# Kernel optimization log

Hardware: AMD Instinct MI355X
Metric: run time of the kernel (lower is better)

## Reference

```python
import jax, jax.numpy as jnp
import numpy as np

Bsz, T, D = 2, 2048, 1024
H_ATTN, HD, WIN = 16, 64, 128
H_SSM, DI, N, DCONV, DTR = 8, 2048, 16, 4, 64
P = DI // H_SSM
DT_MIN, DT_MAX = 1e-4, 1.0
EPS = 1e-6


def setup_inputs() -> dict:
    key = jax.random.key(0)
    ks = jax.random.split(key, 16)
    def g(i, shp, s=0.02):
        return jax.random.normal(ks[i], shp, jnp.float32) * s
    TOT = 2 * DI + DTR + 2 * H_SSM * N
    # dt_bias = inverse_softplus(dt) with dt log-uniform in [dt_min, dt_max]
    dt0 = jnp.exp(jax.random.uniform(ks[14], (H_SSM,), jnp.float32) * (np.log(DT_MAX) - np.log(DT_MIN)) + np.log(DT_MIN))
    dt_bias = dt0 + jnp.log(-jnp.expm1(-dt0))
    return dict(
        x=jax.random.normal(ks[0], (Bsz, T, D), jnp.float32),
        norm1_w=jnp.ones((D,), jnp.float32),
        norm2_w=jnp.ones((D,), jnp.float32),
        Win=g(1, (TOT, D)),
        Wdt=g(2, (H_SSM, DTR)),
        conv_w=g(3, (DI, DCONV), 0.2),
        conv_b=jnp.zeros((DI,), jnp.float32),
        A_log=jnp.log(jnp.broadcast_to(jnp.arange(1, N + 1, dtype=jnp.float32), (H_SSM, N))),
        Dskip=jnp.ones((H_SSM, P), jnp.float32),
        dt_bias=dt_bias,
        ssd_norm_w=jnp.ones((DI,), jnp.float32),
        Wout_ssd=g(4, (D, DI)),
        Wres=g(5, (DI, D)),
        Wq=g(6, (D, D)), Wk=g(7, (D, D)), Wv=g(8, (D, D)), Wo=g(9, (D, D)),
    )


def _rms(x, w):
    return x * jax.lax.rsqrt(jnp.mean(x * x, -1, keepdims=True) + EPS) * w


def _silu(x):
    return x * jax.nn.sigmoid(x)


def _dwconv(x, w, b):
    # causal depthwise conv1d: x [B,T,C], w [C,K], left-pad K-1
    K = w.shape[1]
    xp = jnp.pad(x, ((0, 0), (K - 1, 0), (0, 0)))
    y = sum(xp[:, k:k + x.shape[1], :] * w[:, k] for k in range(K))
    return y + b


def _rope(q, k):
    # q,k: [B,H,T,HD]
    inv = 1.0 / (10000.0 ** (jnp.arange(0, HD, 2, dtype=jnp.float32) / HD))
    t = jnp.arange(q.shape[2], dtype=jnp.float32)
    f = jnp.concatenate([t[:, None] * inv, t[:, None] * inv], -1)  # [T,HD]
    cos, sin = jnp.cos(f), jnp.sin(f)
    def rot(x):
        h = x.shape[-1] // 2
        return jnp.concatenate([-x[..., h:], x[..., :h]], -1)
    return q * cos + rot(q) * sin, k * cos + rot(k) * sin


def _ssd_branch(u, Win, Wdt, conv_w, conv_b, A_log, Dskip, dt_bias, ssd_norm_w, Wout_ssd, Wres):
    B = u.shape[0]
    proj = u @ Win.T  # [B,T,4416]
    xin = proj[..., :DI]
    z = proj[..., DI:2 * DI]
    dtl = proj[..., 2 * DI:2 * DI + DTR]
    o = 2 * DI + DTR
    Bm = proj[..., o:o + H_SSM * N].reshape(B, T, H_SSM, N)
    Cm = proj[..., o + H_SSM * N:].reshape(B, T, H_SSM, N)
    xc = _silu(_dwconv(xin, conv_w, conv_b))
    dt = jnp.clip(jax.nn.softplus(dtl @ Wdt.T + dt_bias), DT_MIN, DT_MAX)  # [B,T,H]
    A = -jnp.exp(A_log)  # [H,N]
    xh = xc.reshape(B, T, H_SSM, P)
    dA = jnp.exp(dt[..., None] * A)  # [B,T,H,N]
    dtB = dt[..., None] * Bm        # [B,T,H,N]

    def step(h, inp):
        dA_t, dtB_t, x_t, C_t = inp
        h = h * dA_t[:, :, None, :] + x_t[..., None] * dtB_t[:, :, None, :]
        y = jnp.einsum('bhpn,bhn->bhp', h, C_t)
        return h, y

    h0 = jnp.zeros((B, H_SSM, P, N), u.dtype)
    _, ys = jax.lax.scan(step, h0, (
        dA.transpose(1, 0, 2, 3), dtB.transpose(1, 0, 2, 3),
        xh.transpose(1, 0, 2, 3), Cm.transpose(1, 0, 2, 3)))
    y = ys.transpose(1, 0, 2, 3) + Dskip * xh  # [B,T,H,P]
    y = y.reshape(B, T, DI) + u @ Wres.T       # residual_proj(d_model->d_inner)
    y = _rms(y * _silu(z), ssd_norm_w)         # fused gated RMSNorm
    return y @ Wout_ssd.T


def _attn(u, Wq, Wk, Wv, Wo):
    B = u.shape[0]
    q = (u @ Wq.T).reshape(B, T, H_ATTN, HD).transpose(0, 2, 1, 3)
    k = (u @ Wk.T).reshape(B, T, H_ATTN, HD).transpose(0, 2, 1, 3)
    v = (u @ Wv.T).reshape(B, T, H_ATTN, HD).transpose(0, 2, 1, 3)
    q, k = _rope(q, k)
    s = jnp.einsum('bhtd,bhsd->bhts', q, k) / np.sqrt(HD).astype(np.float32)
    rel = jnp.arange(T)[:, None] - jnp.arange(T)[None, :]
    allowed = (rel >= 0) & (rel < WIN)  # causal sliding window
    s = jnp.where(allowed, s, jnp.float32(-1e30))
    p = jax.nn.softmax(s, axis=-1)
    y = jnp.einsum('bhts,bhsd->bhtd', p, v)
    return y.transpose(0, 2, 1, 3).reshape(B, T, D) @ Wo.T


def reference(x, norm1_w, norm2_w, Win, Wdt, conv_w, conv_b, A_log, Dskip, dt_bias,
              ssd_norm_w, Wout_ssd, Wres, Wq, Wk, Wv, Wo):
    h = x + _ssd_branch(_rms(x, norm1_w), Win, Wdt, conv_w, conv_b, A_log, Dskip,
                        dt_bias, ssd_norm_w, Wout_ssd, Wres)
    return h + _attn(_rms(h, norm2_w), Wq, Wk, Wv, Wo)
```

## Files before the change

kernel.cpp:

```cpp
#include <hip/hip_runtime.h>
#include <stdint.h>

typedef unsigned short u16;
typedef unsigned int u32;
typedef __attribute__((ext_vector_type(8))) short short8;
typedef __attribute__((ext_vector_type(4))) unsigned short ushort4v;
typedef __attribute__((ext_vector_type(4))) float f32x4;

#define Bsz 2
#define Tn 2048
#define Dm 1024
#define H_ATTN 16
#define HDx 64
#define WINx 128
#define H_SSM 8
#define DIx 2048
#define Nst 16
#define DTRx 64
#define Px 256
#define TOTx 4416
#define TOT2 6464
#define RESOFF 4416
#define OFFC (2*DIx+DTRx+H_SSM*Nst)
#define BT (Bsz*Tn)
#define NCH 32
#define LCH 64

__device__ __forceinline__ float b2f(u16 u){ u32 x = ((u32)u)<<16; float f; __builtin_memcpy(&f,&x,4); return f; }
__device__ __forceinline__ u16 f2b(float f){ u32 x; __builtin_memcpy(&x,&f,4); u32 r = x + 0x7fffu + ((x>>16)&1u); return (u16)(r>>16); }

__device__ __forceinline__ float block_sum256(float v){
  #pragma unroll
  for (int o=32;o;o>>=1) v += __shfl_xor(v,o,64);
  __shared__ float sb[4];
  int wid = threadIdx.x>>6;
  if ((threadIdx.x&63)==0) sb[wid]=v;
  __syncthreads();
  v = sb[0]+sb[1]+sb[2]+sb[3];
  __syncthreads();
  return v;
}

__device__ __forceinline__ void gload_lds16(const void* g, void* l){
  __builtin_amdgcn_global_load_lds((const __attribute__((address_space(1))) void*)g,
                                   (__attribute__((address_space(3))) void*)l, 16, 0, 0);
}

struct CvtArgs { const float* s[7]; u16* d[7]; int n[7]; };
__global__ __launch_bounds__(256) void k_cvt_all(CvtArgs a, int total4){
  int i = blockIdx.x*256 + threadIdx.x;
  if (i >= total4) return;
  int e = i*4;
  #pragma unroll
  for (int j=0;j<7;j++){
    if (e < a.n[j]){
      float4 v = *(const float4*)(a.s[j]+e);
      u16* d = a.d[j]+e;
      d[0]=f2b(v.x); d[1]=f2b(v.y); d[2]=f2b(v.z); d[3]=f2b(v.w);
      return;
    }
    e -= a.n[j];
  }
}

__global__ __launch_bounds__(256) void k_rms1024(const float* __restrict__ src, const float* __restrict__ w,
                                                 u16* __restrict__ dst){
  int row = blockIdx.x, tid = threadIdx.x;
  const float* s = src + (size_t)row*1024;
  float v[4]; float ss=0.f;
  #pragma unroll
  for (int i=0;i<4;i++){ v[i] = s[tid + i*256]; ss += v[i]*v[i]; }
  ss = block_sum256(ss);
  float sc = rsqrtf(ss*(1.0f/1024.0f) + 1e-6f);
  u16* d = dst + (size_t)row*1024;
  #pragma unroll
  for (int i=0;i<4;i++){ int c = tid+i*256; d[c] = f2b(v[i]*sc*w[c]); }
}

#define BKq 64

__global__ __launch_bounds__(512,1)
void k_gemm256(const u16* __restrict__ A, const u16* __restrict__ W,
               u16* __restrict__ C16, int M, int N, int K, int gxx){
  __shared__ u16 lds[2][4][128*64];
  int tid = threadIdx.x, lane = tid&63, wid = tid>>6;
  int bid = blockIdx.x;
  int xcd = bid&7, r = bid>>3;
  int halfg = gxx>>1;
  int row0 = (xcd>>1)<<2, col0 = (xcd&1)*halfg;
  int bx = col0 + (r>>2), by = row0 + (r&3);
  int bm = by*256, bn = bx*256;
  int wr = wid>>2, wcn = wid&3;
  int fr = lane&15, fq = lane>>4;
  f32x4 acc[2][2][4][2];
  #pragma unroll
  for (int a=0;a<2;a++)
    #pragma unroll
    for (int b=0;b<2;b++)
      #pragma unroll
      for (int c=0;c<4;c++)
        #pragma unroll
        for (int d=0;d<2;d++)
          #pragma unroll
          for (int rr=0;rr<4;rr++) acc[a][b][c][d][rr]=0.f;

  auto stageHalf = [&](int b, int q, int tt){
    int k0 = tt*BKq;
    #pragma unroll
    for (int i=0;i<2;i++){
      int idx = i*512 + tid;
      int row = idx>>3, c8 = idx&7;
      const u16* src; int gr;
      if (q < 2){ gr = bm + q*128 + row;     if (gr > M-1) gr = M-1; src = A; }
      else      { gr = bn + (q-2)*128 + row; if (gr > N-1) gr = N-1; src = W; }
      gload_lds16(src + (size_t)gr*K + k0 + ((c8 ^ (row&7)))*8, &lds[b][q][(size_t)idx*8]);
    }
  };
  auto loadA = [&](const u16* aP, short8 (&af)[2][4]){
    #pragma unroll
    for (int kk=0;kk<2;kk++)
      #pragma unroll
      for (int mi=0;mi<4;mi++){
        int row = wr*64 + mi*16 + fr;
        af[kk][mi] = *(const short8*)(aP + row*64 + ((kk*4+fq) ^ (row&7))*8);
      }
  };
  auto loadB = [&](const u16* bP, short8 (&bf)[2][2]){
    #pragma unroll
    for (int kk=0;kk<2;kk++)
      #pragma unroll
      for (int ni=0;ni<2;ni++){
        int row = wcn*32 + ni*16 + fr;
        bf[kk][ni] = *(const short8*)(bP + row*64 + ((kk*4+fq) ^ (row&7))*8);
      }
  };

  int NT = K/BKq;
  stageHalf(0,0,0); stageHalf(0,2,0); stageHalf(0,3,0); stageHalf(0,1,0);

  short8 af[2][4], bf0[2][2], bf1[2][2];
  for (int t=0;t<NT;t++){
    int cb = t&1, nb = cb^1;
    int tn = (t+1 < NT) ? t+1 : t;
    const u16* A0 = &lds[cb][0][0];
    const u16* A1 = &lds[cb][1][0];
    const u16* B0 = &lds[cb][2][0];
    const u16* B1 = &lds[cb][3][0];
    stageHalf(nb,0,tn);
    asm volatile("s_waitcnt vmcnt(6)" ::: "memory");
    __builtin_amdgcn_sched_barrier(0);
    __builtin_amdgcn_s_barrier();
    loadA(A0, af); loadB(B0, bf0);
    asm volatile("s_waitcnt lgkmcnt(0)" ::: "memory");
    __builtin_amdgcn_sched_barrier(0);
    __builtin_amdgcn_s_setprio(1);
    #pragma unroll
    for (int kk=0;kk<2;kk++)
      #pragma unroll
      for (int mi=0;mi<4;mi++)
        #pragma unroll
        for (int ni=0;ni<2;ni++)
          acc[0][0][mi][ni] = __builtin_amdgcn_mfma_f32_16x16x32_bf16(af[kk][mi], bf0[kk][ni], acc[0][0][mi][ni], 0,0,0);
    __builtin_amdgcn_s_setprio(0);
    __builtin_amdgcn_s_barrier();
    stageHalf(nb,2,tn);
    asm volatile("s_waitcnt vmcnt(6)" ::: "memory");
    __builtin_amdgcn_sched_barrier(0);
    __builtin_amdgcn_s_barrier();
    loadB(B1, bf1);
    asm volatile("s_waitcnt lgkmcnt(0)" ::: "memory");
    __builtin_amdgcn_sched_barrier(0);
    __builtin_amdgcn_s_setprio(1);
    #pragma unroll
    for (int kk=0;kk<2;kk++)
      #pragma unroll
      for (int mi=0;mi<4;mi++)
        #pragma unroll
        for (int ni=0;ni<2;ni++)
          acc[0][1][mi][ni] = __builtin_amdgcn_mfma_f32_16x16x32_bf16(af[kk][mi], bf1[kk][ni], acc[0][1][mi][ni], 0,0,0);
    __builtin_amdgcn_s_setprio(0);
    __builtin_amdgcn_s_barrier();
    stageHalf(nb,3,tn);
    asm volatile("s_waitcnt vmcnt(6)" ::: "memory");
    __builtin_amdgcn_sched_barrier(0);
    __builtin_amdgcn_s_barrier();
    loadA(A1, af);
    asm volatile("s_waitcnt lgkmcnt(0)" ::: "memory");
    __builtin_amdgcn_sched_barrier(0);
    __builtin_amdgcn_s_setprio(1);
    #pragma unroll
    for (int kk=0;kk<2;kk++)
      #pragma unroll
      for (int mi=0;mi<4;mi++)
        #pragma unroll
        for (int ni=0;ni<2;ni++)
          acc[1][1][mi][ni] = __builtin_amdgcn_mfma_f32_16x16x32_bf16(af[kk][mi], bf1[kk][ni], acc[1][1][mi][ni], 0,0,0);
    __builtin_amdgcn_s_setprio(0);
    __builtin_amdgcn_s_barrier();
    stageHalf(nb,1,tn);
    asm volatile("s_waitcnt vmcnt(6)" ::: "memory");
    __builtin_amdgcn_sched_barrier(0);
    __builtin_amdgcn_s_barrier();
    __builtin_amdgcn_s_setprio(1);
    #pragma unroll
    for (int kk=0;kk<2;kk++)
      #pragma unroll
      for (int mi=0;mi<4;mi++)
        #pragma unroll
        for (int ni=0;ni<2;ni++)
          acc[1][0][mi][ni] = __builtin_amdgcn_mfma_f32_16x16x32_bf16(af[kk][mi], bf0[kk][ni], acc[1][0][mi][ni], 0,0,0);
    __builtin_amdgcn_s_setprio(0);
    __builtin_amdgcn_s_barrier();
  }
  #pragma unroll
  for (int mh=0;mh<2;mh++)
    #pragma unroll
    for (int nh=0;nh<2;nh++)
      #pragma unroll
      for (int mi=0;mi<4;mi++)
        #pragma unroll
        for (int ni=0;ni<2;ni++){
          int row0o = bm + mh*128 + wr*64 + mi*16 + fq*4;
          int col  = bn + nh*128 + wcn*32 + ni*16 + fr;
          if (col < N){
            #pragma unroll
            for (int rr=0;rr<4;rr++)
              C16[(size_t)(row0o+rr)*N + col] = f2b(acc[mh][nh][mi][ni][rr]);
          }
        }
}

template<int NWC>
__global__ __launch_bounds__(256, (NWC==2?2:3))
void k_gemm(const u16* __restrict__ A, const u16* __restrict__ W,
            float* __restrict__ C, u16* __restrict__ C16, const u16* __restrict__ ADD16,
            u16* __restrict__ qro, u16* __restrict__ kro, u16* __restrict__ vro,
            int M, int N, int K, int gx, int mode){
  constexpr int BN    = 64*NWC;
  constexpr int ROWS  = 128 + BN;
  constexpr int NLOADS= ROWS/32;
  constexpr int MFRAG = (NWC==2)?4:2;
  __shared__ u16 lds[2][ROWS*64];
  int tid = threadIdx.x, lane = tid&63, wid = tid>>6;
  int nwg = gridDim.x;
  int cpx = nwg>>3;
  int bid = blockIdx.x;
  int swz = (bid&7)*cpx + (bid>>3);
  int fourgx = gx<<2;
  int super = swz / fourgx;
  int r     = swz % fourgx;
  int bx = r >> 2;
  int by = (super<<2) + (r&3);
  int bm = by*128, bn = bx*BN;
  int wc = (NWC==2) ? (wid&1) : 0;
  int wr = (NWC==2) ? (wid>>1) : wid;
  int fr = lane&15, fq = lane>>4;
  int s7 = fr&7;
  f32x4 acc[MFRAG][4];
  #pragma unroll
  for (int mi=0;mi<MFRAG;mi++)
    #pragma unroll
    for (int ni=0;ni<4;ni++)
      #pragma unroll
      for (int rr=0;rr<4;rr++) acc[mi][ni][rr]=0.f;

  auto stage = [&](int buf, int t){
    int k0 = t*BKq;
    #pragma unroll
    for (int i=0;i<NLOADS;i++){
      int chunk = i*256 + tid;
      int row = chunk>>3, c8 = chunk&7;
      const u16* src;
      if (row < 128){ int ra = bm + row; if (ra > M-1) ra = M-1; src = A + (size_t)ra*K; }
      else          { int rb = bn + row-128; if (rb > N-1) rb = N-1; src = W + (size_t)rb*K; }
      gload_lds16(src + k0 + ((c8 ^ (row&7)))*8, &lds[buf][(size_t)chunk*8]);
    }
  };

  int NT = K/BKq;
  stage(0, 0);
  stage(1, 1);
  for (int t=0;t<NT;t++){
    int cur = t&1;
    if (t+1 < NT){
      if constexpr (NWC==2) asm volatile("s_waitcnt vmcnt(8)" ::: "memory");
      else                  asm volatile("s_waitcnt vmcnt(6)" ::: "memory");
    } else {
      asm volatile("s_waitcnt vmcnt(0)" ::: "memory");
    }
    __builtin_amdgcn_sched_barrier(0);
    __builtin_amdgcn_s_barrier();
    #pragma unroll
    for (int kk=0;kk<2;kk++){
      short8 bf4[4], af4[MFRAG];
      int slotb = ((kk*4 + fq) ^ s7)*8;
      #pragma unroll
      for (int ni=0;ni<4;ni++)
        bf4[ni] = *(const short8*)(&lds[cur][(128 + wc*64 + ni*16 + fr)*64 + slotb]);
      #pragma unroll
      for (int mi=0;mi<MFRAG;mi++)
        af4[mi] = *(const short8*)(&lds[cur][(wr*(MFRAG*16) + mi*16 + fr)*64 + slotb]);
      #pragma unroll
      for (int mi=0;mi<MFRAG;mi++)
        #pragma unroll
        for (int ni=0;ni<4;ni++)
          acc[mi][ni] = __builtin_amdgcn_mfma_f32_16x16x32_bf16(af4[mi], bf4[ni], acc[mi][ni], 0,0,0);
    }
    asm volatile("s_waitcnt lgkmcnt(0)" ::: "memory");
    __builtin_amdgcn_sched_barrier(0);
    __builtin_amdgcn_s_barrier();
    if (t+2 < NT) stage(cur, t+2);
  }
  if (mode == 5){
    int sec = bn >> 10;
    int hh  = (bn >> 6) & 15;
    #pragma unroll
    for (int mi=0;mi<MFRAG;mi++){
      #pragma unroll
      for (int rr=0;rr<4;rr++){
        int row = bm + wr*(MFRAG*16) + mi*16 + fq*4 + rr;
        int tt = row & (Tn-1), bb = row >> 11;
        size_t dstb = (((size_t)bb*H_ATTN + hh)*Tn + tt)*64;
        if (sec == 2){
          #pragma unroll
          for (int ni=0;ni<4;ni++)
            vro[dstb + ni*16 + fr] = f2b(acc[mi][ni][rr]);
        } else {
          u16* dst = (sec==0) ? qro : kro;
          #pragma unroll
          for (int ni=0;ni<2;ni++){
            int dh = ni*16 + fr;
            float ang = (float)tt * exp2f(-(float)dh * (13.287712379549449f/32.0f));
            float cs = cosf(ang), sn = sinf(ang);
            float lo = acc[mi][ni][rr], hi = acc[mi][ni+2][rr];
            dst[dstb + dh]      = f2b(lo*cs - hi*sn);
            dst[dstb + dh + 32] = f2b(hi*cs + lo*sn);
          }
        }
      }
    }
    return;
  }
  #pragma unroll
  for (int mi=0;mi<MFRAG;mi++){
    int row0 = bm + wr*(MFRAG*16) + mi*16 + fq*4;
    #pragma unroll
    for (int ni=0;ni<4;ni++){
      int col = bn + wc*64 + ni*16 + fr;
      if (col < N){
        #pragma unroll
        for (int rr=0;rr<4;rr++){
          size_t idx = (size_t)(row0+rr)*N + col;
          float v = acc[mi][ni][rr];
          if (mode == 0)      C[idx] = v;
          else if (mode == 2) C16[idx] = f2b(v);
          else                C[idx] = b2f(ADD16[idx]) + v;
        }
      }
    }
  }
}

__global__ __launch_bounds__(256) void k_scan1(
    const u16* __restrict__ proj, const float* __restrict__ Wdt,
    const float* __restrict__ dt_bias, const float* __restrict__ A_log,
    const float* __restrict__ cw, const float* __restrict__ cb,
    const float* __restrict__ Dskip,
    float* __restrict__ expS, u16* __restrict__ y, float* __restrict__ LS){
  __shared__ float sA[1024], sS[1024], sB[1024], sC[1024];
  int bx = blockIdx.x;
  int c = bx & 31, h = (bx>>5)&7, b = bx>>8;
  int tid = threadIdx.x;
  size_t t0 = (size_t)b*Tn + c*64;
  int j = tid>>2, q = tid&3, n0 = q*4;
  {
    const u16* dtl = proj + (t0+j)*TOT2 + 2*DIx + q*16;
    short8 d0 = *(const short8*)(dtl);
    short8 d1 = *(const short8*)(dtl+8);
    const float* wrow = Wdt + h*64 + q*16;
    float part = 0.f;
    #pragma unroll
    for (int e=0;e<8;e++){ part += b2f((u16)d0[e])*wrow[e]; part += b2f((u16)d1[e])*wrow[8+e]; }
    part += __shfl_xor(part, 1, 64);
    part += __shfl_xor(part, 2, 64);
    float v = part + dt_bias[h];
    float sp = (v > 20.0f) ? v : log1pf(expf(v));
    float dt = fminf(fmaxf(sp, 1e-4f), 1.0f);
    ushort4v bm4 = *(const ushort4v*)(proj + (t0+j)*TOT2 + 2*DIx + DTRx + h*16 + n0);
    ushort4v cm4 = *(const ushort4v*)(proj + (t0+j)*TOT2 + OFFC + h*16 + n0);
    #pragma unroll
    for (int i=0;i<4;i++){
      float Av = -expf(A_log[h*16 + n0 + i]);
      sA[j*16+n0+i] = dt*Av;
      sB[j*16+n0+i] = dt*b2f(bm4[i]);
      sC[j*16+n0+i] = b2f(cm4[i]);
    }
  }
  __syncthreads();
  if (tid < 16){
    float cum = 0.f;
    for (int jj=0;jj<64;jj++){ cum += sA[jj*16+tid]; sS[jj*16+tid] = cum; }
  }
  __syncthreads();
  {
    float e[4], s4[4];
    #pragma unroll
    for (int i=0;i<4;i++){ e[i] = expf(sA[j*16+n0+i]); s4[i] = expf(sS[j*16+n0+i]); }
    #pragma unroll
    for (int i=0;i<4;i++){ sA[j*16+n0+i] = e[i]; sS[j*16+n0+i] = s4[i]; }
    float4 ev; ev.x=s4[0]; ev.y=s4[1]; ev.z=s4[2]; ev.w=s4[3];
    *(float4*)(expS + (t0+j)*128 + h*16 + n0) = ev;
  }
  __syncthreads();
  float st[16];
  #pragma unroll
  for (int n=0;n<16;n++) st[n]=0.f;
  int ch = h*Px + tid;
  const u16* pxin = proj + t0*TOT2 + ch;
  const u16* pres = proj + t0*TOT2 + RESOFF + ch;
  float w0=cw[ch*4+0], w1=cw[ch*4+1], w2=cw[ch*4+2], w3=cw[ch*4+3];
  float bcv = cb[ch];
  float dsk = Dskip[ch];
  float x3=0.f, x2=0.f, x1=0.f;
  if (c > 0){
    x3 = b2f(pxin[-(ptrdiff_t)3*TOT2]);
    x2 = b2f(pxin[-(ptrdiff_t)2*TOT2]);
    x1 = b2f(pxin[-(ptrdiff_t)TOT2]);
  }
  u16* yp = y + t0*DIx + ch;
  for (int jj=0;jj<64;jj++){
    float x0 = b2f(pxin[(size_t)jj*TOT2]);
    float cv = bcv + x3*w0 + x2*w1 + x1*w2 + x0*w3;
    float x = cv / (1.0f + expf(-cv));
    x3=x2; x2=x1; x1=x0;
    float acc = b2f(pres[(size_t)jj*TOT2]) + dsk*x;
    #pragma unroll
    for (int n=0;n<16;n++){ st[n] = st[n]*sA[jj*16+n] + x*sB[jj*16+n]; acc += st[n]*sC[jj*16+n]; }
    yp[(size_t)jj*DIx] = f2b(acc);
  }
  float* ls = LS + ((((size_t)b*8+h)*NCH + c)*Px + tid)*16;
  #pragma unroll
  for (int n=0;n<16;n++) ls[n] = st[n];
}

__global__ __launch_bounds__(256) void k_scan2(const float* __restrict__ expS, const float* __restrict__ LS,
                                               float* __restrict__ H0){
  int blk = blockIdx.x;
  int slice = blk & 15;
  int bh = blk >> 4; int b = bh>>3, h = bh&7;
  int tid = threadIdx.x;
  int ch = slice*16 + (tid>>4);
  int n  = tid & 15;
  float Hs = 0.f;
  for (int c=0;c<NCH;c++){
    float dl = expS[((size_t)b*Tn + c*64 + 63)*128 + h*16 + n];
    size_t base = ((((size_t)b*8+h)*NCH + c)*Px + ch)*16 + n;
    H0[base] = Hs;
    Hs = Hs*dl + LS[base];
  }
}

__global__ __launch_bounds__(256) void k_scan3(const u16* __restrict__ proj, const float* __restrict__ expS,
    const float* __restrict__ H0, u16* __restrict__ y){
  __shared__ float ce[1024];
  int bx = blockIdx.x; int c = bx&31, h=(bx>>5)&7, b=bx>>8;
  int tid = threadIdx.x;
  size_t t0 = (size_t)b*Tn + c*64;
  int j = tid>>2, n0=(tid&3)*4;
  {
    ushort4v cv = *(const ushort4v*)(proj + (t0+j)*TOT2 + OFFC + h*16 + n0);
    float4 evv = *(const float4*)(expS + (t0+j)*128 + h*16 + n0);
    ce[j*16+n0+0] = b2f(cv[0])*evv.x; ce[j*16+n0+1] = b2f(cv[1])*evv.y;
    ce[j*16+n0+2] = b2f(cv[2])*evv.z; ce[j*16+n0+3] = b2f(cv[3])*evv.w;
  }
  __syncthreads();
  float h0[16];
  size_t base = ((((size_t)b*8+h)*NCH + c)*Px + tid)*16;
  #pragma unroll
  for (int n=0;n<16;n++) h0[n] = H0[base+n];
  int ch = h*Px + tid;
  u16* yp = y + t0*DIx + ch;
  for (int jj=0;jj<64;jj++){
    float f = 0.f;
    #pragma unroll
    for (int n=0;n<16;n++) f += ce[jj*16+n]*h0[n];
    size_t yi = (size_t)jj*DIx;
    yp[yi] = f2b(b2f(yp[yi]) + f);
  }
}

__global__ __launch_bounds__(256) void k_gatedrms(const u16* __restrict__ y, const u16* __restrict__ proj,
     const float* __restrict__ w, u16* __restrict__ yn){
  int row = blockIdx.x, tid = threadIdx.x;
  const u16* yr = y + (size_t)row*DIx;
  const u16* zr = proj + (size_t)row*TOT2 + DIx;
  float v[8]; float ss=0.f;
  #pragma unroll
  for (int i=0;i<8;i++){
    int cidx = tid + i*256;
    float z = b2f(zr[cidx]);
    float g = b2f(yr[cidx]) * (z / (1.0f + expf(-z)));
    v[i]=g; ss += g*g;
  }
  ss = block_sum256(ss);
  float sc = rsqrtf(ss*(1.0f/2048.0f) + 1e-6f);
  u16* d = yn + (size_t)row*DIx;
  #pragma unroll
  for (int i=0;i<8;i++){ int cidx=tid+i*256; d[cidx] = f2b(v[i]*sc*w[cidx]); }
}

__global__ __launch_bounds__(256) void k_addrms(const float* __restrict__ x, const u16* __restrict__ sout16,
     const float* __restrict__ w, u16* __restrict__ hb16, u16* __restrict__ u2){
  int row=blockIdx.x, tid=threadIdx.x;
  float v[4]; float ss=0.f;
  #pragma unroll
  for (int i=0;i<4;i++){
    int cidx = tid + i*256;
    size_t idx = (size_t)row*1024 + cidx;
    float hv = x[idx] + b2f(sout16[idx]);
    hb16[idx] = f2b(hv);
    v[i]=hv; ss+=hv*hv;
  }
  ss = block_sum256(ss);
  float sc = rsqrtf(ss*(1.0f/1024.0f)+1e-6f);
  #pragma unroll
  for (int i=0;i<4;i++){ int cidx=tid+i*256; u2[(size_t)row*1024+cidx] = f2b(v[i]*sc*w[cidx]); }
}

#define QT 64
#define KSPAN 192
__device__ __forceinline__ u32 swz128a(int row, int b){
  return (u32)((row*128 + b) ^ ((((row&7)^((row>>3)&7)))<<4));
}
__device__ __forceinline__ u32 swz384a(int row, int b){
  return (u32)((row*384 + b) ^ ((((row&7)^((row>>3)&7)))<<4));
}

__global__ __launch_bounds__(256) void k_attn_mfma(const u16* __restrict__ qr, const u16* __restrict__ kr,
    const u16* __restrict__ vr, u16* __restrict__ ya){
  __shared__ u16 bufK[KSPAN*64];
  __shared__ u16 bufV[64*KSPAN];
  int tid = threadIdx.x, lane = tid&63, wid = tid>>6;
  int fr = lane&15, fq = lane>>4;
  int blk = blockIdx.x;
  int qt = blk & 31, bh = blk >> 5;
  int t0 = qt*QT;
  size_t rowbase = (size_t)bh*Tn;
  char* cK = (char*)bufK;
  char* cV = (char*)bufV;

  #pragma unroll
  for (int it=0; it<6; ++it){
    int chunk = it*256 + tid;
    int row = chunk>>3, c8 = chunk&7;
    int sg = t0 - 128 + row;
    if (sg >= 0){
      short8 v = *(const short8*)(kr + (rowbase+sg)*64 + c8*8);
      *(short8*)(cK + swz128a(row, c8*16)) = v;
    }
  }
  #pragma unroll
  for (int it=0; it<6; ++it){
    int idx = it*256 + tid;
    int s = idx>>3, c8 = idx&7, d0 = c8*8;
    int sg = t0 - 128 + s;
    short8 v;
    if (sg >= 0) v = *(const short8*)(vr + (rowbase+sg)*64 + d0);
    else         v = short8{0,0,0,0,0,0,0,0};
    #pragma unroll
    for (int e=0;e<8;e++)
      *(u16*)(cV + swz384a(d0+e, s*2)) = (u16)v[e];
  }
  __syncthreads();

  f32x4 acc[12];
  #pragma unroll
  for (int j=0;j<12;j++)
    #pragma unroll
    for (int r=0;r<4;r++) acc[j][r]=0.f;
  #pragma unroll
  for (int kk=0;kk<2;kk++){
    short8 aq = *(const short8*)(qr + (rowbase + t0 + wid*16 + fr)*64 + kk*32 + fq*8);
    #pragma unroll
    for (int j=0;j<12;j++){
      short8 bk = *(const short8*)(cK + swz128a(j*16+fr, kk*64 + fq*16));
      acc[j] = __builtin_amdgcn_mfma_f32_16x16x32_bf16(aq, bk, acc[j], 0,0,0);
    }
  }

  float p[12][4];
  int cb = lane&15;
  #pragma unroll
  for (int r=0;r<4;r++){
    int rq = wid*16 + (lane>>4)*4 + r;
    float m = -3.0e38f;
    #pragma unroll
    for (int j=0;j<12;j++){
      int c = j*16 + cb;
      bool allowed = (c > rq) && (c <= rq+128) && (c >= 128 - t0);
      float v = allowed ? acc[j][r]*0.125f : -3.0e38f;
      p[j][r] = v;
      m = fmaxf(m, v);
    }
    #pragma unroll
    for (int o=1;o<16;o<<=1) m = fmaxf(m, __shfl_xor(m, o, 64));
    float sum = 0.f;
    #pragma unroll
    for (int j=0;j<12;j++){ float e = __expf(p[j][r]-m); p[j][r]=e; sum += e; }
    #pragma unroll
    for (int o=1;o<16;o<<=1) sum += __shfl_xor(sum, o, 64);
    float inv = 1.0f/sum;
    #pragma unroll
    for (int j=0;j<12;j++) p[j][r] *= inv;
  }
  __syncthreads();

  #pragma unroll
  for (int r=0;r<4;r++){
    int rq = wid*16 + (lane>>4)*4 + r;
    #pragma unroll
    for (int j=0;j<12;j++){
      *(u16*)(cK + swz384a(rq, (j*16+cb)*2)) = f2b(p[j][r]);
    }
  }
  __syncthreads();

  f32x4 acc2[4];
  #pragma unroll
  for (int f=0;f<4;f++)
    #pragma unroll
    for (int r=0;r<4;r++) acc2[f][r]=0.f;
  #pragma unroll
  for (int kk=0;kk<6;kk++){
    short8 ap = *(const short8*)(cK + swz384a(wid*16 + fr, kk*64 + fq*16));
    #pragma unroll
    for (int f=0;f<4;f++){
      short8 bv = *(const short8*)(cV + swz384a(f*16+fr, kk*64 + fq*16));
      acc2[f] = __builtin_amdgcn_mfma_f32_16x16x32_bf16(ap, bv, acc2[f], 0,0,0);
    }
  }
  int b = bh >> 4, h = bh & 15;
  #pragma unroll
  for (int f=0;f<4;f++){
    int d = f*16 + cb;
    #pragma unroll
    for (int r=0;r<4;r++){
      int q = t0 + wid*16 + (lane>>4)*4 + r;
      ya[((size_t)b*Tn + q)*Dm + h*64 + d] = f2b(acc2[f][r]);
    }
  }
}

extern "C" void kernel_launch(void* const* d_in, const int* in_sizes, int n_in,
                              void* d_out, int out_size, void* d_ws, size_t ws_size,
                              hipStream_t stream) {
  const float* x        = (const float*)d_in[0];
  const float* norm1_w  = (const float*)d_in[1];
  const float* norm2_w  = (const float*)d_in[2];
  const float* Win      = (const float*)d_in[3];
  const float* Wdt      = (const float*)d_in[4];
  const float* conv_w   = (const float*)d_in[5];
  const float* conv_b   = (const float*)d_in[6];
  const float* A_log    = (const float*)d_in[7];
  const float* Dskip    = (const float*)d_in[8];
  const float* dt_bias  = (const float*)d_in[9];
  const float* ssd_norm = (const float*)d_in[10];
  const float* Wout_ssd = (const float*)d_in[11];
  const float* Wres     = (const float*)d_in[12];
  const float* Wq       = (const float*)d_in[13];
  const float* Wk       = (const float*)d_in[14];
  const float* Wv       = (const float*)d_in[15];
  const float* Wo       = (const float*)d_in[16];

  char* ws = (char*)d_ws;
  size_t off = 0;
  auto alloc = [&](size_t bytes){ size_t r = off; off += (bytes + 255) & ~(size_t)255; return r; };

  size_t o_WinB  = alloc((size_t)TOTx*Dm*2);
  size_t o_WresB = alloc((size_t)DIx*Dm*2);
  size_t o_WoutB = alloc((size_t)Dm*DIx*2);
  size_t o_WqB   = alloc((size_t)Dm*Dm*2);
  size_t o_WkB   = alloc((size_t)Dm*Dm*2);
  size_t o_WvB   = alloc((size_t)Dm*Dm*2);
  size_t o_WoB   = alloc((size_t)Dm*Dm*2);
  size_t o_u1    = alloc((size_t)BT*Dm*2);
  size_t o_proj  = alloc((size_t)BT*TOT2*2);
  size_t o_sout  = alloc((size_t)BT*Dm*2);
  size_t o_expS  = alloc((size_t)BT*H_SSM*Nst*4);
  size_t o_LS    = alloc((size_t)Bsz*H_SSM*NCH*Px*Nst*4);
  size_t o_H0    = alloc((size_t)Bsz*H_SSM*NCH*Px*Nst*4);
  size_t o_y     = alloc((size_t)BT*DIx*2);
  size_t o_yn    = alloc((size_t)BT*DIx*2);
  size_t o_hb    = alloc((size_t)BT*Dm*2);
  size_t o_qr    = alloc((size_t)Bsz*H_ATTN*Tn*HDx*2);
  size_t o_kr    = alloc((size_t)Bsz*H_ATTN*Tn*HDx*2);

  u16* WinB  = (u16*)(ws + o_WinB);
  u16* WoutB = (u16*)(ws + o_WoutB);
  u16* WqB   = (u16*)(ws + o_WqB);
  u16* u1    = (u16*)(ws + o_u1);
  u16* projb = (u16*)(ws + o_proj);
  float* expS = (float*)(ws + o_expS);
  float* LS   = (float*)(ws + o_LS);
  float* H0   = (float*)(ws + o_H0);
  u16*   ybuf16 = (u16*)(ws + o_y);
  u16*   yn   = (u16*)(ws + o_yn);
  u16*   hb16 = (u16*)(ws + o_hb);
  u16*   sout16 = (u16*)(ws + o_sout);
  u16* qr = (u16*)(ws + o_qr);
  u16* kr = (u16*)(ws + o_kr);
  u16* vr = u1;
  u16* yatt = (u16*)(ws + o_y);

  {
    CvtArgs a;
    a.s[0]=Win;  a.d[0]=WinB;  a.n[0]=TOTx*Dm;
    a.s[1]=Wres; a.d[1]=(u16*)(ws + o_WresB); a.n[1]=DIx*Dm;
    a.s[2]=Wout_ssd; a.d[2]=WoutB; a.n[2]=Dm*DIx;
    a.s[3]=Wq; a.d[3]=WqB; a.n[3]=Dm*Dm;
    a.s[4]=Wk; a.d[4]=(u16*)(ws + o_WkB); a.n[4]=Dm*Dm;
    a.s[5]=Wv; a.d[5]=(u16*)(ws + o_WvB); a.n[5]=Dm*Dm;
    a.s[6]=Wo; a.d[6]=(u16*)(ws + o_WoB); a.n[6]=Dm*Dm;
    int total4 = (a.n[0]+a.n[1]+a.n[2]+a.n[3]+a.n[4]+a.n[5]+a.n[6])/4;
    k_cvt_all<<<dim3((total4+255)/256), dim3(256), 0, stream>>>(a, total4);
  }

  k_rms1024<<<dim3(BT), dim3(256), 0, stream>>>(x, norm1_w, u1);
  k_gemm256<<<dim3(16*26), dim3(512), 0, stream>>>(u1, WinB, projb, BT, TOT2, Dm, 26);
  k_scan1<<<dim3(Bsz*H_SSM*NCH), dim3(256), 0, stream>>>(projb, Wdt, dt_bias, A_log,
                                                         conv_w, conv_b, Dskip, expS, ybuf16, LS);
  k_scan2<<<dim3(Bsz*H_SSM*16), dim3(256), 0, stream>>>(expS, LS, H0);
  k_scan3<<<dim3(Bsz*H_SSM*NCH), dim3(256), 0, stream>>>(projb, expS, H0, ybuf16);
  k_gatedrms<<<dim3(BT), dim3(256), 0, stream>>>(ybuf16, projb, ssd_norm, yn);
  k_gemm<1><<<dim3(16*32), dim3(256), 0, stream>>>(yn, WoutB, nullptr, sout16, nullptr,
                                                   nullptr, nullptr, nullptr, BT, Dm, DIx, 16, 2);
  k_addrms<<<dim3(BT), dim3(256), 0, stream>>>(x, sout16, norm2_w, hb16, (u16*)(ws + o_yn));
  u16* u2p = (u16*)(ws + o_yn);
  k_gemm<1><<<dim3(48*32), dim3(256), 0, stream>>>(u2p, WqB, nullptr, nullptr, nullptr,
                                                   qr, kr, vr, BT, 3*Dm, Dm, 48, 5);
  k_attn_mfma<<<dim3(Bsz*H_ATTN*(Tn/QT)), dim3(256), 0, stream>>>(qr, kr, vr, yatt);
  k_gemm<1><<<dim3(16*32), dim3(256), 0, stream>>>(yatt, (u16*)(ws + o_WoB), (float*)d_out, nullptr, hb16,
                                                   nullptr, nullptr, nullptr, BT, Dm, Dm, 16, 3);
  (void)in_sizes; (void)n_in; (void)out_size; (void)ws_size;
}
```

Baseline: 271.6 us.

## Stage scan inputs through LDS and move residual add into gated RMSNorm

k_scan1 now copies the 64x256 block of conv inputs into shared memory with 16-byte global-to-LDS loads, replacing the strided per-timestep 2-byte global reads. k_scan3 stages its y tile in LDS, updates it there, and writes it back as vectorized short8 stores. The residual projection add moves from scan1 into k_gatedrms, where it is read as coalesced rows. The cost is 32KB of extra LDS per block, which may lower occupancy. The residual is now added after the bf16 rounding of y rather than in fp32 inside the scan, so results can differ slightly.

```diff
diff --git a/kernel.cpp b/kernel.cpp
--- a/kernel.cpp
+++ b/kernel.cpp
@@ -368,11 +368,18 @@
     const float* __restrict__ Dskip,
     float* __restrict__ expS, u16* __restrict__ y, float* __restrict__ LS){
   __shared__ float sA[1024], sS[1024], sB[1024], sC[1024];
+  __shared__ u16 xt[64*256];
   int bx = blockIdx.x;
   int c = bx & 31, h = (bx>>5)&7, b = bx>>8;
   int tid = threadIdx.x;
   size_t t0 = (size_t)b*Tn + c*64;
   int j = tid>>2, q = tid&3, n0 = q*4;
+  #pragma unroll
+  for (int i=0;i<8;i++){
+    int chunk = i*256 + tid;
+    int row = chunk>>5, col8 = (chunk&31)*8;
+    gload_lds16(proj + (t0+row)*TOT2 + h*Px + col8, &xt[(size_t)chunk*8]);
+  }
   {
     const u16* dtl = proj + (t0+j)*TOT2 + 2*DIx + q*16;
     short8 d0 = *(const short8*)(dtl);
@@ -417,7 +424,6 @@
   for (int n=0;n<16;n++) st[n]=0.f;
   int ch = h*Px + tid;
   const u16* pxin = proj + t0*TOT2 + ch;
-  const u16* pres = proj + t0*TOT2 + RESOFF + ch;
   float w0=cw[ch*4+0], w1=cw[ch*4+1], w2=cw[ch*4+2], w3=cw[ch*4+3];
   float bcv = cb[ch];
   float dsk = Dskip[ch];
@@ -429,11 +435,11 @@
   }
   u16* yp = y + t0*DIx + ch;
   for (int jj=0;jj<64;jj++){
-    float x0 = b2f(pxin[(size_t)jj*TOT2]);
+    float x0 = b2f(xt[jj*256 + tid]);
     float cv = bcv + x3*w0 + x2*w1 + x1*w2 + x0*w3;
     float x = cv / (1.0f + expf(-cv));
     x3=x2; x2=x1; x1=x0;
-    float acc = b2f(pres[(size_t)jj*TOT2]) + dsk*x;
+    float acc = dsk*x;
     #pragma unroll
     for (int n=0;n<16;n++){ st[n] = st[n]*sA[jj*16+n] + x*sB[jj*16+n]; acc += st[n]*sC[jj*16+n]; }
     yp[(size_t)jj*DIx] = f2b(acc);
@@ -463,10 +469,17 @@
 __global__ __launch_bounds__(256) void k_scan3(const u16* __restrict__ proj, const float* __restrict__ expS,
     const float* __restrict__ H0, u16* __restrict__ y){
   __shared__ float ce[1024];
+  __shared__ u16 yt[64*256];
   int bx = blockIdx.x; int c = bx&31, h=(bx>>5)&7, b=bx>>8;
   int tid = threadIdx.x;
   size_t t0 = (size_t)b*Tn + c*64;
   int j = tid>>2, n0=(tid&3)*4;
+  #pragma unroll
+  for (int i=0;i<8;i++){
+    int chunk = i*256 + tid;
+    int row = chunk>>5, col8 = (chunk&31)*8;
+    gload_lds16(y + (t0+row)*DIx + h*Px + col8, &yt[(size_t)chunk*8]);
+  }
   {
     ushort4v cv = *(const ushort4v*)(proj + (t0+j)*TOT2 + OFFC + h*16 + n0);
     float4 evv = *(const float4*)(expS + (t0+j)*128 + h*16 + n0);
@@ -478,14 +491,19 @@
   size_t base = ((((size_t)b*8+h)*NCH + c)*Px + tid)*16;
   #pragma unroll
   for (int n=0;n<16;n++) h0[n] = H0[base+n];
-  int ch = h*Px + tid;
-  u16* yp = y + t0*DIx + ch;
   for (int jj=0;jj<64;jj++){
     float f = 0.f;
     #pragma unroll
     for (int n=0;n<16;n++) f += ce[jj*16+n]*h0[n];
-    size_t yi = (size_t)jj*DIx;
-    yp[yi] = f2b(b2f(yp[yi]) + f);
+    int li = jj*256 + tid;
+    yt[li] = f2b(b2f(yt[li]) + f);
+  }
+  __syncthreads();
+  #pragma unroll
+  for (int i=0;i<8;i++){
+    int chunk = i*256 + tid;
+    int row = chunk>>5, col8 = (chunk&31)*8;
+    *(short8*)(y + (t0+row)*DIx + h*Px + col8) = *(const short8*)(&yt[(size_t)chunk*8]);
   }
 }
 
@@ -494,12 +512,13 @@
   int row = blockIdx.x, tid = threadIdx.x;
   const u16* yr = y + (size_t)row*DIx;
   const u16* zr = proj + (size_t)row*TOT2 + DIx;
+  const u16* rr = proj + (size_t)row*TOT2 + RESOFF;
   float v[8]; float ss=0.f;
   #pragma unroll
   for (int i=0;i<8;i++){
     int cidx = tid + i*256;
     float z = b2f(zr[cidx]);
-    float g = b2f(yr[cidx]) * (z / (1.0f + expf(-z)));
+    float g = (b2f(yr[cidx]) + b2f(rr[cidx])) * (z / (1.0f + expf(-z)));
     v[i]=g; ss += g*g;
   }
   ss = block_sum256(ss);
```

New measurement: 274.6 us. About the same (+1.1%).
